# Kernel tuning notes

Hardware: AMD Instinct MI355X
Metric: run time of the kernel (lower is better)

The kernel has to match this reference:

```python
import jax, jax.numpy as jnp
import numpy as np


def _rope(x, pos, theta):
    # x: [b, s, h, d], pos: [s] int. Standard interleaved RoPE on even/odd pairs.
    d = x.shape[-1]
    inv_freq = theta ** (-jnp.arange(0, d, 2, dtype=jnp.float32) / d)  # [d/2]
    ang = pos.astype(jnp.float32)[:, None] * inv_freq                  # [s, d/2]
    cos = jnp.cos(ang)[None, :, None, :]
    sin = jnp.sin(ang)[None, :, None, :]
    x1 = x[..., 0::2]
    x2 = x[..., 1::2]
    rot = jnp.stack([x1 * cos - x2 * sin, x1 * sin + x2 * cos], axis=-1)
    return rot.reshape(x.shape)


def setup_inputs() -> dict:
    key = jax.random.key(0)
    ks = jax.random.split(key, 5)
    b, s, d = 4, 2048, 1024
    scale = 1.0 / np.sqrt(d)
    return {
        "x": jax.random.normal(ks[0], (b, s, d), dtype=jnp.float32),
        "W_Q": jax.random.normal(ks[1], (d, d), dtype=jnp.float32) * scale,
        "W_K": jax.random.normal(ks[2], (d, d), dtype=jnp.float32) * scale,
        "W_V": jax.random.normal(ks[3], (d, d), dtype=jnp.float32) * scale,
        "W_O": jax.random.normal(ks[4], (d, d), dtype=jnp.float32) * scale,
        "token_positions": jnp.arange(s, dtype=jnp.int32),
    }


def reference(x, W_Q, W_K, W_V, W_O, token_positions):
    num_heads = 16
    theta = 10000.0
    b, s, d_model = x.shape
    d_k = d_model // num_heads

    Q = x @ W_Q.T  # [b, s, d_model]
    K = x @ W_K.T
    V = x @ W_V.T

    # split heads: last dim is [h0 | h1 | ...] so reshape to [b, s, h, d_k]
    Qh = Q.reshape(b, s, num_heads, d_k)
    Kh = K.reshape(b, s, num_heads, d_k)
    Vh = V.reshape(b, s, num_heads, d_k)

    Qh = _rope(Qh, token_positions, theta)
    Kh = _rope(Kh, token_positions, theta)

    scores = jnp.einsum("bqhd,bkhd->bhqk", Qh, Kh) / jnp.sqrt(
        jnp.asarray(d_k, dtype=x.dtype)
    )
    causal = jnp.tril(jnp.ones((s, s), dtype=bool))  # True = keep
    scores = jnp.where(causal[None, None, :, :], scores, jnp.asarray(-jnp.inf, x.dtype))
    probs = jax.nn.softmax(scores, axis=-1)

    out = jnp.einsum("bhqk,bkhd->bqhd", probs, Vh).reshape(b, s, d_model)
    return out @ W_O.T
```

## Files before the change

kernel.cpp:

```cpp
#include <hip/hip_runtime.h>
#include <hip/hip_bf16.h>
#include <type_traits>

typedef __attribute__((ext_vector_type(8))) short short8;
typedef __attribute__((ext_vector_type(4))) short s16x4;
typedef __attribute__((ext_vector_type(4))) float f32x4;
typedef unsigned short u16;
typedef unsigned int   u32;
typedef unsigned long long u64;


#if __has_builtin(__builtin_amdgcn_mfma_f32_16x16x16bf16_1k)
#define MFMA16(a, b, c) __builtin_amdgcn_mfma_f32_16x16x16bf16_1k(a, b, c, 0, 0, 0)
#define HAVE_MFMA16 1
#elif __has_builtin(__builtin_amdgcn_mfma_f32_16x16x16_bf16)
#define MFMA16(a, b, c) __builtin_amdgcn_mfma_f32_16x16x16_bf16(a, b, c, 0, 0, 0)
#define HAVE_MFMA16 1
#else
#define HAVE_MFMA16 0
#endif

static __device__ __forceinline__ u16 f2b(float f) {
  u32 u = __builtin_bit_cast(u32, f);
  u = (u + 0x7fffu + ((u >> 16) & 1u)) >> 16;
  return (u16)u;
}
static __device__ __forceinline__ float b2f(u16 h) {
  return __builtin_bit_cast(float, ((u32)h) << 16);
}
static __device__ __forceinline__ u32 pkbf(float a, float b) {
  union { __hip_bfloat162 t; u32 u; } c;
  c.t = __float22bfloat162_rn(make_float2(a, b));
  return c.u;
}

typedef __attribute__((address_space(1))) const unsigned int gas_u32;
typedef __attribute__((address_space(3))) unsigned int las_u32;
static __device__ __forceinline__ void glds16(const u16* g, u16* l) {
  __builtin_amdgcn_global_load_lds((gas_u32*)g, (las_u32*)l, 16, 0, 0);
}

__global__ __launch_bounds__(256) void cvt_all(
    const float* __restrict__ x, const float* __restrict__ wq,
    const float* __restrict__ wk, const float* __restrict__ wv,
    const float* __restrict__ wo, u16* __restrict__ xb, u16* __restrict__ wqb,
    u16* __restrict__ wkb, u16* __restrict__ wvb, u16* __restrict__ wob) {
  int u = blockIdx.x * 256 + threadIdx.x;
  if (u >= 3145728) return;
  const float* src; u16* dst; int off;
  if (u < 2097152) { src = x; dst = xb; off = u; }
  else {
    int t = u - 2097152;
    int w = t >> 18;
    off = t & 0x3FFFF;
    src = (w == 0) ? wq : (w == 1) ? wk : (w == 2) ? wv : wo;
    dst = (w == 0) ? wqb : (w == 1) ? wkb : (w == 2) ? wvb : wob;
  }
  int i = off * 4;
  float4 v = *(const float4*)(src + i);
  union { u16 us[4]; u64 ull; } o;
  o.us[0] = f2b(v.x); o.us[1] = f2b(v.y); o.us[2] = f2b(v.z); o.us[3] = f2b(v.w);
  *(u64*)(dst + i) = o.ull;
}

template <typename OT>
static __device__ __forceinline__ void gemm_body(const u16* __restrict__ A,
                                                 const u16* __restrict__ B,
                                                 OT* __restrict__ C,
                                                 int m0, int n0) {
  __shared__ u16 As[4096];
  __shared__ u16 Bs[4096];

  const int tid  = threadIdx.x;
  const int lane = tid & 63;
  const int wv   = tid >> 6;
  const int quad = lane >> 4;
  const int cc   = lane & 15;
  const int wr   = wv >> 1;
  const int wc   = wv & 1;

  f32x4 acc[4][4];
#pragma unroll
  for (int i = 0; i < 4; i++)
#pragma unroll
    for (int j = 0; j < 4; j++) acc[i][j] = (f32x4){0.f, 0.f, 0.f, 0.f};

  const int p0 = wv * 128 + lane;
  const int p1 = p0 + 64;
  const int r0 = p0 >> 2, g0 = (p0 & 3) ^ (r0 & 3);
  const int r1 = p1 >> 2, g1 = (p1 & 3) ^ (r1 & 3);
  const u16* gA0 = A + (size_t)(m0 + r0) * 1024 + g0 * 8;
  const u16* gA1 = A + (size_t)(m0 + r1) * 1024 + g1 * 8;
  const u16* gB0 = B + (size_t)(n0 + r0) * 1024 + g0 * 8;
  const u16* gB1 = B + (size_t)(n0 + r1) * 1024 + g1 * 8;
  u16* lA = As + wv * 1024;
  u16* lB = Bs + wv * 1024;

  for (int k0 = 0; k0 < 1024; k0 += 32) {
    __syncthreads();
    glds16(gA0 + k0, lA);
    glds16(gA1 + k0, lA + 512);
    glds16(gB0 + k0, lB);
    glds16(gB1 + k0, lB + 512);
    __syncthreads();

    short8 af[4], bf[4];
#pragma unroll
    for (int mt = 0; mt < 4; mt++) {
      int ra = wr * 64 + mt * 16 + cc;
      af[mt] = *(const short8*)&As[ra * 32 + ((quad ^ (ra & 3)) * 8)];
    }
#pragma unroll
    for (int nt = 0; nt < 4; nt++) {
      int rb = wc * 64 + nt * 16 + cc;
      bf[nt] = *(const short8*)&Bs[rb * 32 + ((quad ^ (rb & 3)) * 8)];
    }
#pragma unroll
    for (int mt = 0; mt < 4; mt++)
#pragma unroll
      for (int nt = 0; nt < 4; nt++)
        acc[mt][nt] = __builtin_amdgcn_mfma_f32_16x16x32_bf16(af[mt], bf[nt], acc[mt][nt], 0, 0, 0);
  }

#pragma unroll
  for (int mt = 0; mt < 4; mt++)
#pragma unroll
    for (int nt = 0; nt < 4; nt++)
#pragma unroll
      for (int r = 0; r < 4; r++) {
        int row = m0 + wr * 64 + mt * 16 + quad * 4 + r;
        int col = n0 + wc * 64 + nt * 16 + cc;
        if constexpr (std::is_same_v<OT, float>)
          C[(size_t)row * 1024 + col] = acc[mt][nt][r];
        else
          C[(size_t)row * 1024 + col] = f2b(acc[mt][nt][r]);
      }
}

__global__ __launch_bounds__(256) void gemm_qkv(const u16* __restrict__ A,
                                                const u16* __restrict__ Bq,
                                                const u16* __restrict__ Bk,
                                                const u16* __restrict__ Bv,
                                                u16* __restrict__ Q,
                                                u16* __restrict__ K,
                                                u16* __restrict__ V) {
  int sel = blockIdx.x >> 3;
  const u16* B = (sel == 0) ? Bq : (sel == 1) ? Bk : Bv;
  u16* C = (sel == 0) ? Q : (sel == 1) ? K : V;
  gemm_body<u16>(A, B, C, blockIdx.y * 128, (blockIdx.x & 7) * 128);
}

__global__ __launch_bounds__(256) void gemm_out(const u16* __restrict__ A,
                                                const u16* __restrict__ B,
                                                float* __restrict__ C) {
  gemm_body<float>(A, B, C, blockIdx.y * 128, blockIdx.x * 128);
}

__global__ __launch_bounds__(256) void rope_kernel(u16* __restrict__ Q,
                                                   u16* __restrict__ K,
                                                   const int* __restrict__ pos) {
  u16* T = blockIdx.y ? K : Q;
  const float sc = blockIdx.y ? 1.0f : 0.125f;
  int idx = blockIdx.x * 256 + threadIdx.x;
  int row = idx >> 9;
  int p   = idx & 511;
  int i   = p & 31;
  int col = (p >> 5) * 64 + 2 * i;
  int s   = row & 2047;
  float ps  = (float)pos[s];
  float inv = exp2f(-(float)i * 0.41524101186092033f);
  float ang = ps * inv;
  float sn, cs;
  sincosf(ang, &sn, &cs);
  u32 v = *(u32*)(T + (size_t)row * 1024 + col);
  float x1 = b2f((u16)(v & 0xffffu));
  float x2 = b2f((u16)(v >> 16));
  float y1 = (x1 * cs - x2 * sn) * sc;
  float y2 = (x1 * sn + x2 * cs) * sc;
  *(u32*)(T + (size_t)row * 1024 + col) = (u32)f2b(y1) | ((u32)f2b(y2) << 16);
}

__global__ __launch_bounds__(256) void transpose_v(const u16* __restrict__ V,
                                                   u16* __restrict__ Vt) {
  __shared__ u16 t[64][65];
  int s0 = blockIdx.x * 64;
  int bh = blockIdx.y;
  int b = bh >> 4, h = bh & 15;
  int tid = threadIdx.x;
  int r = tid >> 2, ch = (tid & 3) * 16;
  const u16* src = V + (size_t)(b * 2048 + s0 + r) * 1024 + h * 64 + ch;
  union { uint4 v[2]; u16 us[16]; } tmp;
  tmp.v[0] = *(const uint4*)src;
  tmp.v[1] = *(const uint4*)(src + 8);
#pragma unroll
  for (int j = 0; j < 16; j++) t[r][ch + j] = tmp.us[j];
  __syncthreads();
  union { uint4 v[2]; u16 us[16]; } o;
#pragma unroll
  for (int j = 0; j < 16; j++) o.us[j] = t[ch + j][r];
  u16* dst = Vt + (size_t)(bh * 64 + r) * 2048 + s0 + ch;
  *(uint4*)dst = o.v[0];
  *(uint4*)(dst + 8) = o.v[1];
}

__global__ __launch_bounds__(256) void attn_kernel(const u16* __restrict__ Q,
                                                   const u16* __restrict__ K,
                                                   const u16* __restrict__ Vt,
                                                   u16* __restrict__ O) {
  __shared__ u16 Ks[8192];
  __shared__ u16 Vs[8192];
#if !HAVE_MFMA16
  __shared__ u16 Ps[4 * 16 * 136];
#endif

  const int bh = blockIdx.x;
  const int qt = 15 - blockIdx.y;
  const int b = bh >> 4, h = bh & 15;
  const int tid  = threadIdx.x;
  const int lane = tid & 63;
  const int wv   = tid >> 6;
  const int quad = lane >> 4;
  const int cc   = lane & 15;
  const int q0   = qt * 128;

  short8 qf[2][2];
#pragma unroll
  for (int mt = 0; mt < 2; mt++) {
    const u16* qp = Q + (size_t)(b * 2048 + q0 + wv * 32 + mt * 16 + cc) * 1024 + h * 64;
    qf[mt][0] = *(const short8*)(qp + quad * 8);
    qf[mt][1] = *(const short8*)(qp + 32 + quad * 8);
  }

  f32x4 o_acc[2][4];
  float m_i[2] = {-3.0e38f, -3.0e38f}, l_i[2] = {0.f, 0.f};
#pragma unroll
  for (int mt = 0; mt < 2; mt++)
#pragma unroll
    for (int nt = 0; nt < 4; nt++) o_acc[mt][nt] = (f32x4){0.f, 0.f, 0.f, 0.f};

  const u16* Kp = K + ((size_t)(b * 2048) + wv * 32 + (lane >> 3)) * 1024 + h * 64 +
                  (((lane & 7) ^ (lane >> 3)) * 8);
  const u16* Vp[4];
#pragma unroll
  for (int j = 0; j < 4; j++) {
    int rl = wv * 16 + j * 4 + (lane >> 4);
    int g  = ((lane & 15) - rl) & 15;
    Vp[j] = Vt + ((size_t)(bh * 64) + rl) * 2048 + g * 8;
  }

  const int nkt = qt + 1;
  const int pk0 = (quad ^ (cc & 7)) * 8;

  for (int kt = 0; kt < nkt; ++kt) {
    __syncthreads();
#pragma unroll
    for (int j = 0; j < 4; j++) {
      glds16(Kp + (size_t)kt * 131072 + j * 8192, Ks + wv * 2048 + j * 512);
      glds16(Vp[j] + kt * 128, Vs + wv * 2048 + j * 512);
    }
    __syncthreads();

    const bool diag = (kt == qt);

#pragma unroll
    for (int mt = 0; mt < 2; ++mt) {
      f32x4 s[8];
#pragma unroll
      for (int nt = 0; nt < 8; ++nt) {
        const int rbase = (nt * 16 + cc) * 64;
        short8 bk0 = *(const short8*)&Ks[rbase + pk0];
        short8 bk1 = *(const short8*)&Ks[rbase + (pk0 ^ 32)];
        f32x4 z = (f32x4){0.f, 0.f, 0.f, 0.f};
        z = __builtin_amdgcn_mfma_f32_16x16x32_bf16(bk0, qf[mt][0], z, 0, 0, 0);
        s[nt] = __builtin_amdgcn_mfma_f32_16x16x32_bf16(bk1, qf[mt][1], z, 0, 0, 0);
      }

      if (diag) {
        const int qg = q0 + wv * 32 + mt * 16 + cc;
        const int kb = kt * 128 + quad * 4;
#pragma unroll
        for (int nt = 0; nt < 8; ++nt)
#pragma unroll
          for (int r = 0; r < 4; ++r)
            if (kb + nt * 16 + r > qg) s[nt][r] = -3.0e38f;
      }

      float mx = s[0][0];
#pragma unroll
      for (int nt = 0; nt < 8; ++nt)
#pragma unroll
        for (int r = 0; r < 4; ++r) mx = fmaxf(mx, s[nt][r]);
      mx = fmaxf(mx, __shfl_xor(mx, 16));
      mx = fmaxf(mx, __shfl_xor(mx, 32));
      const float mn = fmaxf(m_i[mt], mx);
      const float al = __expf(m_i[mt] - mn);
      m_i[mt] = mn;

      s16x4 pf[8];
      float ps = 0.f;
#pragma unroll
      for (int nt = 0; nt < 8; ++nt) {
        float e0 = __expf(s[nt][0] - mn);
        float e1 = __expf(s[nt][1] - mn);
        float e2 = __expf(s[nt][2] - mn);
        float e3 = __expf(s[nt][3] - mn);
        ps += (e0 + e1) + (e2 + e3);
        union { u32 w[2]; s16x4 v; } pu;
        pu.w[0] = pkbf(e0, e1);
        pu.w[1] = pkbf(e2, e3);
        pf[nt] = pu.v;
      }
      l_i[mt] = l_i[mt] * al + ps;

      f32x4 al4;
#pragma unroll
      for (int r = 0; r < 4; ++r) al4[r] = __shfl(al, quad * 4 + r);
#pragma unroll
      for (int nt = 0; nt < 4; ++nt) o_acc[mt][nt] *= al4;

#if HAVE_MFMA16
#pragma unroll
      for (int nt = 0; nt < 4; ++nt) {
        const int rv = (nt * 16 + cc) * 128;
#pragma unroll
        for (int kk = 0; kk < 8; ++kk) {
          const int pos = (kk * 2 + (quad >> 1) + cc) & 15;
          s16x4 bv = *(const s16x4*)&Vs[rv + pos * 8 + (quad & 1) * 4];
          o_acc[mt][nt] = MFMA16(pf[kk], bv, o_acc[mt][nt]);
        }
      }
#else
#pragma unroll
      for (int nt = 0; nt < 8; ++nt) {
        union { s16x4 v; u64 ull; } pu2; pu2.v = pf[nt];
        *(u64*)&Ps[(wv * 16 + cc) * 136 + nt * 16 + quad * 4] = pu2.ull;
      }
      short8 pa[4];
#pragma unroll
      for (int ks = 0; ks < 4; ++ks)
        pa[ks] = *(const short8*)&Ps[(wv * 16 + cc) * 136 + ks * 32 + quad * 8];
#pragma unroll
      for (int nt = 0; nt < 4; ++nt) {
        const int rv = (nt * 16 + cc) * 128;
#pragma unroll
        for (int ks = 0; ks < 4; ++ks) {
          const int pos = (ks * 4 + quad + cc) & 15;
          short8 bv = *(const short8*)&Vs[rv + pos * 8];
          o_acc[mt][nt] = __builtin_amdgcn_mfma_f32_16x16x32_bf16(pa[ks], bv, o_acc[mt][nt], 0, 0, 0);
        }
      }
#endif
    }
  }

#pragma unroll
  for (int mt = 0; mt < 2; ++mt) {
    float l = l_i[mt];
    l += __shfl_xor(l, 16);
    l += __shfl_xor(l, 32);
    const float linv = 1.0f / l;
    f32x4 li4;
#pragma unroll
    for (int r = 0; r < 4; ++r) li4[r] = __shfl(linv, quad * 4 + r);
    const int rowb = b * 2048 + q0 + wv * 32 + mt * 16 + quad * 4;
#pragma unroll
    for (int nt = 0; nt < 4; ++nt)
#pragma unroll
      for (int r = 0; r < 4; ++r)
        O[(size_t)(rowb + r) * 1024 + h * 64 + nt * 16 + cc] = f2b(o_acc[mt][nt][r] * li4[r]);
  }
}

extern "C" void kernel_launch(void* const* d_in, const int* in_sizes, int n_in,
                              void* d_out, int out_size, void* d_ws, size_t ws_size,
                              hipStream_t stream) {
  const float* x  = (const float*)d_in[0];
  const float* wq = (const float*)d_in[1];
  const float* wk = (const float*)d_in[2];
  const float* wv = (const float*)d_in[3];
  const float* wo = (const float*)d_in[4];
  const int* pos  = (const int*)d_in[5];
  float* out = (float*)d_out;

  char* ws = (char*)d_ws;
  u16* xb  = (u16*)(ws);
  u16* vt  = (u16*)(ws);
  u16* wqb = (u16*)(ws + (16ull << 20));
  u16* wkb = (u16*)(ws + (18ull << 20));
  u16* wvb = (u16*)(ws + (20ull << 20));
  u16* wob = (u16*)(ws + (22ull << 20));
  u16* Qb  = (u16*)(ws + (24ull << 20));
  u16* Kb  = (u16*)(ws + (40ull << 20));
  u16* Vb  = (u16*)(ws + (56ull << 20));
  u16* aO  = Vb;

  cvt_all<<<12288, 256, 0, stream>>>(x, wq, wk, wv, wo, xb, wqb, wkb, wvb, wob);
  gemm_qkv<<<dim3(24, 64), 256, 0, stream>>>(xb, wqb, wkb, wvb, Qb, Kb, Vb);
  rope_kernel<<<dim3(16384, 2), 256, 0, stream>>>(Qb, Kb, pos);
  transpose_v<<<dim3(32, 64), 256, 0, stream>>>(Vb, vt);
  attn_kernel<<<dim3(64, 16), 256, 0, stream>>>(Qb, Kb, vt, aO);
  gemm_out<<<dim3(8, 64), 256, 0, stream>>>(aO, wob, out);
}
```

Measured before the change: 299.5 us.

## Double-buffer K tiles, overlap V loads with QK, and use lazy exp2 softmax rescaling

Prefetches the next K tile into a second shared buffer while the current tile is computed, and issues the V tile load before the QK MFMAs so the load overlaps compute. This removes the barrier-then-load stall at the top of each iteration. Softmax now works in the base-2 domain, with log2(e) folded into the Q scale inside the rope kernel, and skips rescaling O and l unless the running max grows by more than a threshold. It also raises MFMA wave priority and sets a 3-blocks-per-CU launch bound. The cost is extra shared memory and register pressure from computing both score tiles at once, and the threshold trades slightly larger exp values for fewer rescales.

New measurement: 326.2 us. 8.9% more time.

```diff
diff --git a/kernel.cpp b/kernel.cpp
--- a/kernel.cpp
+++ b/kernel.cpp
@@ -160,7 +160,7 @@
                                                    u16* __restrict__ K,
                                                    const int* __restrict__ pos) {
   u16* T = blockIdx.y ? K : Q;
-  const float sc = blockIdx.y ? 1.0f : 0.125f;
+  const float sc = blockIdx.y ? 1.0f : 0.18033688011112042f;
   int idx = blockIdx.x * 256 + threadIdx.x;
   int row = idx >> 9;
   int p   = idx & 511;
@@ -203,11 +203,90 @@
   *(uint4*)(dst + 8) = o.v[1];
 }
 
-__global__ __launch_bounds__(256) void attn_kernel(const u16* __restrict__ Q,
-                                                   const u16* __restrict__ K,
-                                                   const u16* __restrict__ Vt,
-                                                   u16* __restrict__ O) {
-  __shared__ u16 Ks[8192];
+
+#define SOFTMAX_STEP(MT, SV, PF)                                           \
+  do {                                                                     \
+    float mx = fmaxf(fmaxf(SV[0][0], SV[0][1]), fmaxf(SV[0][2], SV[0][3]));\
+    _Pragma("unroll")                                                      \
+    for (int nt = 1; nt < 8; ++nt)                                         \
+      mx = fmaxf(mx, fmaxf(fmaxf(SV[nt][0], SV[nt][1]),                    \
+                           fmaxf(SV[nt][2], SV[nt][3])));                  \
+    mx = fmaxf(mx, __shfl_xor(mx, 16));                                    \
+    mx = fmaxf(mx, __shfl_xor(mx, 32));                                    \
+    if (!__all(mx <= m_i[MT] + 11.0f)) {                                   \
+      const float mn = fmaxf(m_i[MT], mx);                                 \
+      const float al = exp2f(m_i[MT] - mn);                                \
+      m_i[MT] = mn;                                                        \
+      l_i[MT] *= al;                                                       \
+      f32x4 al4;                                                           \
+      _Pragma("unroll")                                                    \
+      for (int r = 0; r < 4; ++r) al4[r] = __shfl(al, quad * 4 + r);       \
+      _Pragma("unroll")                                                    \
+      for (int nt = 0; nt < 4; ++nt) o_acc[MT][nt] *= al4;                 \
+    }                                                                      \
+    const float mu = m_i[MT];                                              \
+    float ps = 0.f;                                                        \
+    _Pragma("unroll")                                                      \
+    for (int nt = 0; nt < 8; ++nt) {                                       \
+      float e0 = exp2f(SV[nt][0] - mu);                                    \
+      float e1 = exp2f(SV[nt][1] - mu);                                    \
+      float e2 = exp2f(SV[nt][2] - mu);                                    \
+      float e3 = exp2f(SV[nt][3] - mu);                                    \
+      ps += (e0 + e1) + (e2 + e3);                                         \
+      union { u32 w[2]; s16x4 v; } pu;                                     \
+      pu.w[0] = pkbf(e0, e1);                                              \
+      pu.w[1] = pkbf(e2, e3);                                              \
+      PF[nt] = pu.v;                                                       \
+    }                                                                      \
+    l_i[MT] += ps;                                                         \
+  } while (0)
+
+#if HAVE_MFMA16
+#define PV_STEP(MT, PF)                                                    \
+  do {                                                                     \
+    __builtin_amdgcn_s_setprio(1);                                         \
+    _Pragma("unroll")                                                      \
+    for (int nt = 0; nt < 4; ++nt) {                                       \
+      const int rv = (nt * 16 + cc) * 128;                                 \
+      _Pragma("unroll")                                                    \
+      for (int kk = 0; kk < 8; ++kk) {                                     \
+        const int pos = (kk * 2 + (quad >> 1) + cc) & 15;                  \
+        s16x4 bv = *(const s16x4*)&Vs[rv + pos * 8 + (quad & 1) * 4];      \
+        o_acc[MT][nt] = MFMA16(PF[kk], bv, o_acc[MT][nt]);                 \
+      }                                                                    \
+    }                                                                      \
+    __builtin_amdgcn_s_setprio(0);                                         \
+  } while (0)
+#else
+#define PV_STEP(MT, PF)                                                    \
+  do {                                                                     \
+    _Pragma("unroll")                                                      \
+    for (int nt = 0; nt < 8; ++nt) {                                       \
+      union { s16x4 v; u64 ull; } pu2; pu2.v = PF[nt];                     \
+      *(u64*)&Ps[(wv * 16 + cc) * 136 + nt * 16 + quad * 4] = pu2.ull;     \
+    }                                                                      \
+    short8 pa[4];                                                          \
+    _Pragma("unroll")                                                      \
+    for (int ks = 0; ks < 4; ++ks)                                         \
+      pa[ks] = *(const short8*)&Ps[(wv * 16 + cc) * 136 + ks * 32 + quad * 8];\
+    _Pragma("unroll")                                                      \
+    for (int nt = 0; nt < 4; ++nt) {                                       \
+      const int rv = (nt * 16 + cc) * 128;                                 \
+      _Pragma("unroll")                                                    \
+      for (int ks = 0; ks < 4; ++ks) {                                     \
+        const int pos = (ks * 4 + quad + cc) & 15;                         \
+        short8 bv = *(const short8*)&Vs[rv + pos * 8];                     \
+        o_acc[MT][nt] = __builtin_amdgcn_mfma_f32_16x16x32_bf16(pa[ks], bv, o_acc[MT][nt], 0, 0, 0); \
+      }                                                                    \
+    }                                                                      \
+  } while (0)
+#endif
+
+__global__ __launch_bounds__(256, 3) void attn_kernel(const u16* __restrict__ Q,
+                                                      const u16* __restrict__ K,
+                                                      const u16* __restrict__ Vt,
+                                                      u16* __restrict__ O) {
+  __shared__ u16 Ks[2][8192];
   __shared__ u16 Vs[8192];
 #if !HAVE_MFMA16
   __shared__ u16 Ps[4 * 16 * 136];
@@ -251,106 +330,63 @@
   const int nkt = qt + 1;
   const int pk0 = (quad ^ (cc & 7)) * 8;
 
+#pragma unroll
+  for (int j = 0; j < 4; j++)
+    glds16(Kp, &Ks[0][wv * 2048 + j * 512]), Kp += 8192;
+  Kp -= 4 * 8192;
+  __syncthreads();
+
   for (int kt = 0; kt < nkt; ++kt) {
+    const int cur = kt & 1;
+
+#pragma unroll
+    for (int j = 0; j < 4; j++)
+      glds16(Vp[j] + kt * 128, Vs + wv * 2048 + j * 512);
+    if (kt + 1 < nkt) {
+#pragma unroll
+      for (int j = 0; j < 4; j++)
+        glds16(Kp + (size_t)(kt + 1) * 131072 + j * 8192,
+               &Ks[cur ^ 1][wv * 2048 + j * 512]);
+    }
+
+    f32x4 s0[8], s1[8];
+    __builtin_amdgcn_s_setprio(1);
+#pragma unroll
+    for (int nt = 0; nt < 8; ++nt) {
+      const int rbase = (nt * 16 + cc) * 64;
+      short8 bk0 = *(const short8*)&Ks[cur][rbase + pk0];
+      short8 bk1 = *(const short8*)&Ks[cur][rbase + (pk0 ^ 32)];
+      f32x4 z0 = (f32x4){0.f, 0.f, 0.f, 0.f};
+      z0 = __builtin_amdgcn_mfma_f32_16x16x32_bf16(bk0, qf[0][0], z0, 0, 0, 0);
+      s0[nt] = __builtin_amdgcn_mfma_f32_16x16x32_bf16(bk1, qf[0][1], z0, 0, 0, 0);
+      f32x4 z1 = (f32x4){0.f, 0.f, 0.f, 0.f};
+      z1 = __builtin_amdgcn_mfma_f32_16x16x32_bf16(bk0, qf[1][0], z1, 0, 0, 0);
+      s1[nt] = __builtin_amdgcn_mfma_f32_16x16x32_bf16(bk1, qf[1][1], z1, 0, 0, 0);
+    }
+    __builtin_amdgcn_s_setprio(0);
+
+    if (kt == qt) {
+      const int kb = kt * 128 + quad * 4;
+      const int qg0 = q0 + wv * 32 + cc;
+#pragma unroll
+      for (int nt = 0; nt < 8; ++nt)
+#pragma unroll
+        for (int r = 0; r < 4; ++r) {
+          if (kb + nt * 16 + r > qg0) s0[nt][r] = -3.0e38f;
+          if (kb + nt * 16 + r > qg0 + 16) s1[nt][r] = -3.0e38f;
+        }
+    }
+
+    s16x4 pf0[8], pf1[8];
+    SOFTMAX_STEP(0, s0, pf0);
+
     __syncthreads();
-#pragma unroll
-    for (int j = 0; j < 4; j++) {
-      glds16(Kp + (size_t)kt * 131072 + j * 8192, Ks + wv * 2048 + j * 512);
-      glds16(Vp[j] + kt * 128, Vs + wv * 2048 + j * 512);
-    }
+
+    PV_STEP(0, pf0);
+    SOFTMAX_STEP(1, s1, pf1);
+    PV_STEP(1, pf1);
+
     __syncthreads();
-
-    const bool diag = (kt == qt);
-
-#pragma unroll
-    for (int mt = 0; mt < 2; ++mt) {
-      f32x4 s[8];
-#pragma unroll
-      for (int nt = 0; nt < 8; ++nt) {
-        const int rbase = (nt * 16 + cc) * 64;
-        short8 bk0 = *(const short8*)&Ks[rbase + pk0];
-        short8 bk1 = *(const short8*)&Ks[rbase + (pk0 ^ 32)];
-        f32x4 z = (f32x4){0.f, 0.f, 0.f, 0.f};
-        z = __builtin_amdgcn_mfma_f32_16x16x32_bf16(bk0, qf[mt][0], z, 0, 0, 0);
-        s[nt] = __builtin_amdgcn_mfma_f32_16x16x32_bf16(bk1, qf[mt][1], z, 0, 0, 0);
-      }
-
-      if (diag) {
-        const int qg = q0 + wv * 32 + mt * 16 + cc;
-        const int kb = kt * 128 + quad * 4;
-#pragma unroll
-        for (int nt = 0; nt < 8; ++nt)
-#pragma unroll
-          for (int r = 0; r < 4; ++r)
-            if (kb + nt * 16 + r > qg) s[nt][r] = -3.0e38f;
-      }
-
-      float mx = s[0][0];
-#pragma unroll
-      for (int nt = 0; nt < 8; ++nt)
-#pragma unroll
-        for (int r = 0; r < 4; ++r) mx = fmaxf(mx, s[nt][r]);
-      mx = fmaxf(mx, __shfl_xor(mx, 16));
-      mx = fmaxf(mx, __shfl_xor(mx, 32));
-      const float mn = fmaxf(m_i[mt], mx);
-      const float al = __expf(m_i[mt] - mn);
-      m_i[mt] = mn;
-
-      s16x4 pf[8];
-      float ps = 0.f;
-#pragma unroll
-      for (int nt = 0; nt < 8; ++nt) {
-        float e0 = __expf(s[nt][0] - mn);
-        float e1 = __expf(s[nt][1] - mn);
-        float e2 = __expf(s[nt][2] - mn);
-        float e3 = __expf(s[nt][3] - mn);
-        ps += (e0 + e1) + (e2 + e3);
-        union { u32 w[2]; s16x4 v; } pu;
-        pu.w[0] = pkbf(e0, e1);
-        pu.w[1] = pkbf(e2, e3);
-        pf[nt] = pu.v;
-      }
-      l_i[mt] = l_i[mt] * al + ps;
-
-      f32x4 al4;
-#pragma unroll
-      for (int r = 0; r < 4; ++r) al4[r] = __shfl(al, quad * 4 + r);
-#pragma unroll
-      for (int nt = 0; nt < 4; ++nt) o_acc[mt][nt] *= al4;
-
-#if HAVE_MFMA16
-#pragma unroll
-      for (int nt = 0; nt < 4; ++nt) {
-        const int rv = (nt * 16 + cc) * 128;
-#pragma unroll
-        for (int kk = 0; kk < 8; ++kk) {
-          const int pos = (kk * 2 + (quad >> 1) + cc) & 15;
-          s16x4 bv = *(const s16x4*)&Vs[rv + pos * 8 + (quad & 1) * 4];
-          o_acc[mt][nt] = MFMA16(pf[kk], bv, o_acc[mt][nt]);
-        }
-      }
-#else
-#pragma unroll
-      for (int nt = 0; nt < 8; ++nt) {
-        union { s16x4 v; u64 ull; } pu2; pu2.v = pf[nt];
-        *(u64*)&Ps[(wv * 16 + cc) * 136 + nt * 16 + quad * 4] = pu2.ull;
-      }
-      short8 pa[4];
-#pragma unroll
-      for (int ks = 0; ks < 4; ++ks)
-        pa[ks] = *(const short8*)&Ps[(wv * 16 + cc) * 136 + ks * 32 + quad * 8];
-#pragma unroll
-      for (int nt = 0; nt < 4; ++nt) {
-        const int rv = (nt * 16 + cc) * 128;
-#pragma unroll
-        for (int ks = 0; ks < 4; ++ks) {
-          const int pos = (ks * 4 + quad + cc) & 15;
-          short8 bv = *(const short8*)&Vs[rv + pos * 8];
-          o_acc[mt][nt] = __builtin_amdgcn_mfma_f32_16x16x32_bf16(pa[ks], bv, o_acc[mt][nt], 0, 0, 0);
-        }
-      }
-#endif
-    }
   }
 
 #pragma unroll
```
